# Kernel optimization log

Hardware: AMD Instinct MI355X
Metric: run time of the kernel (lower is better)

The kernel has to match this reference:

```python
import jax, jax.numpy as jnp
import numpy as np

DEPTH = 3  # node_info_propagator_stack_depth


def _gru_cell(x, h, W_ih, W_hh, b_ih, b_hh):
    # torch.nn.GRUCell math; x = input, h = hidden state
    gx = x @ W_ih.T + b_ih          # [..., 3P]
    gh = h @ W_hh.T + b_hh
    xr, xz, xn = jnp.split(gx, 3, axis=-1)
    hr, hz, hn = jnp.split(gh, 3, axis=-1)
    r = jax.nn.sigmoid(xr + hr)
    z = jax.nn.sigmoid(xz + hz)
    n = jnp.tanh(xn + r * hn)
    return (1.0 - z) * n + z * h


def setup_inputs() -> dict:
    key = jax.random.key(0)
    ks = jax.random.split(key, 16)
    B, N, E, P, C = 16, 4096, 256, 256, 8
    x = jax.random.normal(ks[0], (B, N, E), dtype=jnp.float32)
    parent_idx = jax.random.randint(ks[1], (B, N), 0, N, dtype=jnp.int32)
    children_idx = jax.random.randint(ks[2], (B, N, C), 0, N, dtype=jnp.int32)
    child_count = jax.random.randint(ks[3], (B, N), 1, C + 1, dtype=jnp.int32)

    def w(k, shape, fan_in):
        return jax.random.uniform(k, shape, dtype=jnp.float32,
                                  minval=-1.0, maxval=1.0) / np.sqrt(fan_in)

    return {
        "nodeInfosTensor": x,
        "parent_idx": parent_idx,
        "children_idx": children_idx,
        "child_count": child_count,
        "W_resize": w(ks[4], (P, E), E), "b_resize": w(ks[5], (P,), E),
        "W_parent": w(ks[6], (P, P), P), "b_parent": w(ks[7], (P,), P),
        "W_nbr": w(ks[8], (P, P), P), "b_nbr": w(ks[9], (P,), P),
        "W_ih": w(ks[10], (3 * P, P), P), "W_hh": w(ks[11], (3 * P, P), P),
        "b_ih": w(ks[12], (3 * P,), P), "b_hh": w(ks[13], (3 * P,), P),
    }


def reference(nodeInfosTensor, parent_idx, children_idx, child_count,
              W_resize, b_resize, W_parent, b_parent, W_nbr, b_nbr,
              W_ih, W_hh, b_ih, b_hh):
    h = nodeInfosTensor @ W_resize.T + b_resize          # [B,N,P]
    B, N, P = h.shape
    C = children_idx.shape[-1]
    # mask out padded child slots; original sums real children then /= count
    mask = (jnp.arange(C)[None, None, :] < child_count[:, :, None]).astype(h.dtype)
    inv_count = 1.0 / child_count.astype(h.dtype)        # count >= 1
    flat_children = children_idx.reshape(B, N * C)
    for _ in range(DEPTH):
        parent_info = jnp.take_along_axis(h, parent_idx[:, :, None], axis=1)  # [B,N,P]
        child_info = jnp.take_along_axis(h, flat_children[:, :, None], axis=1)
        child_info = child_info.reshape(B, N, C, P)
        nbr_info = (child_info * mask[..., None]).sum(axis=2) * inv_count[:, :, None]
        summary = (parent_info @ W_parent.T + b_parent) + (nbr_info @ W_nbr.T + b_nbr)
        # gruCell(input=h, hidden=summary)
        h = _gru_cell(h, summary, W_ih, W_hh, b_ih, b_hh)
    return h
```

## Files before the change

kernel.cpp:

```cpp
#include <hip/hip_runtime.h>

typedef unsigned short us;
typedef us us4 __attribute__((ext_vector_type(4)));
typedef us us8 __attribute__((ext_vector_type(8)));
typedef short bf16x8 __attribute__((ext_vector_type(8)));
typedef float f32x4 __attribute__((ext_vector_type(4)));

#define DEVI static __device__ __forceinline__

#define BB 16
#define NN 4096
#define PP 256
#define CC 8
#define MM (BB * NN)

DEVI float bf2f(us u) { unsigned x = ((unsigned)u) << 16; return __builtin_bit_cast(float, x); }
DEVI us f2bf(float f) {
  unsigned x = __builtin_bit_cast(unsigned, f);
  x += 0x7fffu + ((x >> 16) & 1u);
  return (us)(x >> 16);
}

DEVI void gload_lds16(const void* g, void* l) {
  __builtin_amdgcn_global_load_lds(
      (const __attribute__((address_space(1))) void*)g,
      (__attribute__((address_space(3))) void*)l, 16, 0, 0);
}

DEVI float sigf(float x) { return 1.f / (1.f + __expf(-x)); }
DEVI float tanhfast(float a) {
  float aa = fabsf(a);
  float t = 1.f - 2.f / (1.f + __expf(2.f * aa));
  return copysignf(t, a);
}

DEVI void raw_barrier() {
  __builtin_amdgcn_sched_barrier(0);
  __builtin_amdgcn_s_barrier();
  __builtin_amdgcn_sched_barrier(0);
}

__global__ void k_prep(const float* __restrict__ Wres,
                       const float* __restrict__ Wpar, const float* __restrict__ bpar,
                       const float* __restrict__ Wnbr, const float* __restrict__ bnbr,
                       const float* __restrict__ Wih, const float* __restrict__ Whh,
                       const float* __restrict__ bih, const float* __restrict__ bhh,
                       us* __restrict__ Wr, us* __restrict__ Wcat, float* __restrict__ bcat,
                       us* __restrict__ Wgh, us* __restrict__ Wgs, float* __restrict__ bg) {
  int tid = blockIdx.x * blockDim.x + threadIdx.x;
  int nth = gridDim.x * blockDim.x;
  for (int i = tid; i < 256 * 256; i += nth) Wr[i] = f2bf(Wres[i]);
  for (int i = tid; i < 256 * 512; i += nth) {
    int o = i >> 9, k = i & 511;
    float v = (k < 256) ? Wpar[o * 256 + k] : Wnbr[o * 256 + (k - 256)];
    Wcat[i] = f2bf(v);
  }
  for (int i = tid; i < 256; i += nth) bcat[i] = bpar[i] + bnbr[i];
  for (int i = tid; i < 768 * 256; i += nth) {
    int R = i >> 8, k = i & 255;
    int j = (R / 48) * 16 + (R & 15);
    int slot = (R >> 4) % 3;
    Wgh[i] = f2bf(Wih[(size_t)(slot * 256 + j) * 256 + k]);
    Wgs[i] = f2bf(Whh[(size_t)(slot * 256 + j) * 256 + k]);
  }
  for (int i = tid; i < 1024; i += nth) {
    int g = (i >> 4) & 3, j = ((i >> 6) << 4) + (i & 15);
    float v;
    if (g == 0)      v = bih[j] + bhh[j];
    else if (g == 1) v = bih[256 + j] + bhh[256 + j];
    else if (g == 2) v = bih[512 + j];
    else             v = bhh[512 + j];
    bg[i] = v;
  }
}

DEVI void mma8(const us* As, const us* Bs, int wr, int wc, int l,
               f32x4 (&acc)[8][4]) {
#pragma unroll
  for (int ks = 0; ks < 2; ++ks) {
    bf16x8 af[8], bfr[4];
#pragma unroll
    for (int i = 0; i < 8; ++i) {
      int row = wr * 128 + i * 16 + (l & 15);
      int kb = ((ks * 32 + (l >> 4) * 8) * 2) ^ ((row & 7) << 4);
      af[i] = *(const bf16x8*)((const char*)As + row * 128 + kb);
    }
#pragma unroll
    for (int j = 0; j < 4; ++j) {
      int row = wc * 64 + j * 16 + (l & 15);
      int kb = ((ks * 32 + (l >> 4) * 8) * 2) ^ ((row & 7) << 4);
      bfr[j] = *(const bf16x8*)((const char*)Bs + row * 128 + kb);
    }
#pragma unroll
    for (int i = 0; i < 8; ++i)
#pragma unroll
      for (int j = 0; j < 4; ++j)
        acc[i][j] = __builtin_amdgcn_mfma_f32_16x16x32_bf16(af[i], bfr[j], acc[i][j], 0, 0, 0);
  }
}

template <int HN, int KS>
DEVI void mma4g_ks(const us* As, const us* Bs, int wr, int wc, int l,
                   f32x4 (&acc)[4][4]) {
  bf16x8 af[4], bfr[3];
#pragma unroll
  for (int i = 0; i < 4; ++i) {
    int row = wr * 64 + i * 16 + (l & 15);
    int kb = ((KS * 32 + (l >> 4) * 8) * 2) ^ ((row & 7) << 4);
    af[i] = *(const bf16x8*)((const char*)As + row * 128 + kb);
  }
#pragma unroll
  for (int j = 0; j < 3; ++j) {
    int row = wc * 48 + j * 16 + (l & 15);
    int kb = ((KS * 32 + (l >> 4) * 8) * 2) ^ ((row & 7) << 4);
    bfr[j] = *(const bf16x8*)((const char*)Bs + row * 128 + kb);
  }
  __builtin_amdgcn_s_setprio(1);
#pragma unroll
  for (int i = 0; i < 4; ++i)
#pragma unroll
    for (int j = 0; j < 3; ++j) {
      int aj = (j < 2) ? j : (HN ? 3 : 2);
      acc[i][aj] = __builtin_amdgcn_mfma_f32_16x16x32_bf16(af[i], bfr[j], acc[i][aj], 0, 0, 0);
    }
  __builtin_amdgcn_s_setprio(0);
}

__global__ __launch_bounds__(512, 2)
void k_gemm0(const float* __restrict__ x, const us* __restrict__ Bw,
             const float* __restrict__ bias, us* __restrict__ outBf) {
  __shared__ __align__(16) us As[256 * 64];
  __shared__ __align__(16) us Bs[256 * 64];
  int tid = threadIdx.x;
  int w = tid >> 6, l = tid & 63;
  int wr = w >> 2, wc = w & 3;
  int bid = blockIdx.x;
  int per = gridDim.x >> 3;
  int mi = (bid & 7) * per + (bid >> 3);
  int mBase = mi * 256;
  f32x4 acc[8][4] = {};

#pragma unroll
  for (int t = 0; t < 4; ++t) {
    int kt = t * 64;
#pragma unroll
    for (int c = 0; c < 4; ++c) {
      int row = c * 64 + (tid >> 3);
      int kbb = ((tid & 7) * 16) ^ ((row & 7) << 4);
      const float* src = x + (size_t)(mBase + row) * 256 + kt + (kbb >> 1);
      float4 a = *(const float4*)src;
      float4 b = *(const float4*)(src + 4);
      us8 v;
      v[0] = f2bf(a.x); v[1] = f2bf(a.y); v[2] = f2bf(a.z); v[3] = f2bf(a.w);
      v[4] = f2bf(b.x); v[5] = f2bf(b.y); v[6] = f2bf(b.z); v[7] = f2bf(b.w);
      *(us8*)((char*)As + row * 128 + (tid & 7) * 16) = v;
      int kb = ((tid & 7) * 16) ^ ((row & 7) << 4);
      gload_lds16((const char*)(Bw + (size_t)row * 256 + kt) + kb,
                  (char*)Bs + row * 128 + (tid & 7) * 16);
    }
    asm volatile("s_waitcnt vmcnt(0)" ::: "memory");
    __syncthreads();
    mma8(As, Bs, wr, wc, l, acc);
    __syncthreads();
  }

  int rBase0 = mBase + wr * 128;
  int cBase0 = wc * 64;
#pragma unroll
  for (int i = 0; i < 8; ++i)
#pragma unroll
    for (int j = 0; j < 4; ++j) {
      int col = cBase0 + j * 16 + (l & 15);
      int row0 = rBase0 + i * 16 + ((l >> 4) << 2);
      float bb = bias[col];
#pragma unroll
      for (int e = 0; e < 4; ++e)
        outBf[(size_t)(row0 + e) * 256 + col] = f2bf(acc[i][j][e] + bb);
    }
}

__global__ __launch_bounds__(512, 2)
void k_sgemm(const us* __restrict__ h, const int* __restrict__ par,
             const int* __restrict__ chd, const int* __restrict__ cnt,
             const us* __restrict__ Wcat, const float* __restrict__ bcat,
             us* __restrict__ outBf, float* __restrict__ outF, int writeF32) {
  __shared__ __align__(16) us As[2][256 * 64];
  __shared__ __align__(16) us Bs[2][256 * 64];
  int tid = threadIdx.x;
  int w = tid >> 6, l = tid & 63;
  int wr = w >> 2, wc = w & 3;
  int bid = blockIdx.x;
  int per = gridDim.x >> 3;
  int mi = (bid & 7) * per + (bid >> 3);
  int mBase = mi * 256;
  int bb = (mBase >> 12) << 12;
  f32x4 acc[8][4] = {};

  int prow[4];
#pragma unroll
  for (int c = 0; c < 4; ++c)
    prow[c] = bb + par[mBase + c * 64 + (tid >> 3)];

  auto stageB = [&](int t) {
    int kt = t * 64, buf = t & 1;
#pragma unroll
    for (int c = 0; c < 4; ++c) {
      int row = c * 64 + (tid >> 3);
      int kb = ((tid & 7) * 16) ^ ((row & 7) << 4);
      gload_lds16((const char*)(Wcat + (size_t)row * 512 + kt) + kb,
                  (char*)Bs[buf] + row * 128 + (tid & 7) * 16);
    }
  };
  auto stageG = [&](int t) {
    int kt = t * 64, buf = t & 1;
#pragma unroll
    for (int c = 0; c < 4; ++c) {
      int row = c * 64 + (tid >> 3);
      int kb = ((tid & 7) * 16) ^ ((row & 7) << 4);
      gload_lds16((const char*)(h + (size_t)prow[c] * 256 + kt) + kb,
                  (char*)As[buf] + row * 128 + (tid & 7) * 16);
    }
    stageB(t);
  };
  auto stageN = [&](int t) {
    int kt = t * 64, buf = t & 1;
    int kOffBase = kt - 256;
#pragma unroll
    for (int c = 0; c < 4; ++c) {
      int row = c * 64 + (tid >> 3);
      int m = mBase + row;
      int kbb = ((tid & 7) * 16) ^ ((row & 7) << 4);
      const us* hb = h + (size_t)bb * 256 + kOffBase + (kbb >> 1);
      int4 c0 = *(const int4*)(chd + (size_t)m * CC);
      int4 c1 = *(const int4*)(chd + (size_t)m * CC + 4);
      int ci[8] = {c0.x, c0.y, c0.z, c0.w, c1.x, c1.y, c1.z, c1.w};
      int cn = cnt[m];
      float aa[8] = {0.f, 0.f, 0.f, 0.f, 0.f, 0.f, 0.f, 0.f};
#pragma unroll
      for (int r2 = 0; r2 < 2; ++r2) {
        us8 cv[4];
#pragma unroll
        for (int i2 = 0; i2 < 4; ++i2)
          cv[i2] = *(const us8*)(hb + (size_t)ci[r2 * 4 + i2] * 256);
#pragma unroll
        for (int i2 = 0; i2 < 4; ++i2) {
          float wgt = (r2 * 4 + i2 < cn) ? 1.f : 0.f;
#pragma unroll
          for (int e = 0; e < 8; ++e) aa[e] += wgt * bf2f(cv[i2][e]);
        }
      }
      float inv = 1.f / (float)cn;
      us8 nb;
#pragma unroll
      for (int e = 0; e < 8; ++e) nb[e] = f2bf(aa[e] * inv);
      *(us8*)((char*)As[buf] + row * 128 + (tid & 7) * 16) = nb;
    }
    asm volatile("s_waitcnt lgkmcnt(0)" ::: "memory");
    stageB(t);
  };

  stageG(0);
#pragma unroll
  for (int t = 0; t < 8; ++t) {
    if (t + 1 < 8) {
      if (t + 1 < 4) stageG(t + 1);
      else           stageN(t + 1);
    }
    if (t + 1 < 4)      asm volatile("s_waitcnt vmcnt(8)" ::: "memory");
    else if (t < 7)     asm volatile("s_waitcnt vmcnt(4)" ::: "memory");
    else                asm volatile("s_waitcnt vmcnt(0)" ::: "memory");
    raw_barrier();
    mma8(As[t & 1], Bs[t & 1], wr, wc, l, acc);
    raw_barrier();
  }

  int rBase0 = mBase + wr * 128;
  int cBase0 = wc * 64;
#pragma unroll
  for (int i = 0; i < 8; ++i)
#pragma unroll
    for (int j = 0; j < 4; ++j) {
      int col = cBase0 + j * 16 + (l & 15);
      int row0 = rBase0 + i * 16 + ((l >> 4) << 2);
      float bbia = bcat[col];
#pragma unroll
      for (int e = 0; e < 4; ++e) {
        float v = acc[i][j][e] + bbia;
        size_t off = (size_t)(row0 + e) * 256 + col;
        outBf[off] = f2bf(v);
        if (writeF32) outF[off] = v;
      }
    }
}

__global__ __launch_bounds__(512, 2)
void k_gates(const us* __restrict__ h, const us* __restrict__ s,
             const us* __restrict__ Wgh, const us* __restrict__ Wgs,
             const float* __restrict__ bg,
             us* __restrict__ outBf, float* __restrict__ outF,
             const us* __restrict__ svBf, const float* __restrict__ sF,
             int finalIt) {
  __shared__ __align__(16) us As[2][128 * 64];
  __shared__ __align__(16) us Bs[2][192 * 64];
  int tid = threadIdx.x;
  int w = tid >> 6, l = tid & 63;
  int wr = w >> 2, wc = w & 3;
  int bid = blockIdx.x;
  int per = gridDim.x >> 3;
  int g = (bid & 7) * per + (bid >> 3);
  int mi = g >> 2, ni = g & 3;
  int mBase = mi * 128, nB = ni * 192, nBase = ni * 256;
  f32x4 acc[4][4] = {};

  auto stageA = [&](int t) {
    int buf = t & 1;
    const us* aSrc = (t < 4) ? h : s;
    int kOff = (t & 3) * 64;
#pragma unroll
    for (int c = 0; c < 2; ++c) {
      int row = c * 64 + (tid >> 3);
      int kb = ((tid & 7) * 16) ^ ((row & 7) << 4);
      gload_lds16((const char*)(aSrc + (size_t)(mBase + row) * 256 + kOff) + kb,
                  (char*)As[buf] + row * 128 + (tid & 7) * 16);
    }
  };
  auto stageBw = [&](int t) {
    int buf = t & 1;
    const us* bSrc = (t < 4) ? Wgh : Wgs;
    int kOff = (t & 3) * 64;
#pragma unroll
    for (int c = 0; c < 3; ++c) {
      int row = c * 64 + (tid >> 3);
      int kb = ((tid & 7) * 16) ^ ((row & 7) << 4);
      gload_lds16((const char*)(bSrc + (size_t)(nB + row) * 256 + kOff) + kb,
                  (char*)Bs[buf] + row * 128 + (tid & 7) * 16);
    }
  };

  stageA(0); stageBw(0);
#pragma unroll
  for (int t = 0; t < 8; ++t) {
    if (t + 1 < 8) {
      stageA(t + 1); stageBw(t + 1);
      asm volatile("s_waitcnt vmcnt(5)" ::: "memory");
    } else {
      asm volatile("s_waitcnt vmcnt(0)" ::: "memory");
    }
    raw_barrier();
    const us* A = As[t & 1];
    const us* B = Bs[t & 1];
    if (t < 4) {
      mma4g_ks<0, 0>(A, B, wr, wc, l, acc);
      mma4g_ks<0, 1>(A, B, wr, wc, l, acc);
    } else {
      mma4g_ks<1, 0>(A, B, wr, wc, l, acc);
      mma4g_ks<1, 1>(A, B, wr, wc, l, acc);
    }
    raw_barrier();
  }

  int rBase0 = mBase + wr * 64;
  int cB = nBase + wc * 64;
  int outCol = ((nBase >> 6) + wc) * 16 + (l & 15);
  float b0 = bg[cB + 0  + (l & 15)];
  float b1 = bg[cB + 16 + (l & 15)];
  float b2 = bg[cB + 32 + (l & 15)];
  float b3 = bg[cB + 48 + (l & 15)];
#pragma unroll
  for (int i = 0; i < 4; ++i) {
    int row0 = rBase0 + i * 16 + ((l >> 4) << 2);
#pragma unroll
    for (int e = 0; e < 4; ++e) {
      float r = sigf(acc[i][0][e] + b0);
      float z = sigf(acc[i][1][e] + b1);
      float n = tanhfast(acc[i][2][e] + b2 + r * (acc[i][3][e] + b3));
      size_t off = (size_t)(row0 + e) * 256 + outCol;
      float sv = finalIt ? sF[off] : bf2f(svBf[off]);
      float o = (1.f - z) * n + z * sv;
      if (finalIt) outF[off] = o;
      else         outBf[off] = f2bf(o);
    }
  }
}

extern "C" void kernel_launch(void* const* d_in, const int* in_sizes, int n_in,
                              void* d_out, int out_size, void* d_ws, size_t ws_size,
                              hipStream_t stream) {
  const float* x    = (const float*)d_in[0];
  const int*   par  = (const int*)d_in[1];
  const int*   chd  = (const int*)d_in[2];
  const int*   cnt  = (const int*)d_in[3];
  const float* Wres = (const float*)d_in[4];
  const float* bres = (const float*)d_in[5];
  const float* Wpar = (const float*)d_in[6];
  const float* bpar = (const float*)d_in[7];
  const float* Wnbr = (const float*)d_in[8];
  const float* bnbr = (const float*)d_in[9];
  const float* Wih  = (const float*)d_in[10];
  const float* Whh  = (const float*)d_in[11];
  const float* bih  = (const float*)d_in[12];
  const float* bhh  = (const float*)d_in[13];

  char* ws = (char*)d_ws;
  size_t off = 0;
  auto alloc = [&](size_t sz) { char* p = ws + off; off += (sz + 255) & ~(size_t)255; return p; };
  us*    Wgh  = (us*)alloc((size_t)768 * 256 * 2);
  us*    Wgs  = (us*)alloc((size_t)768 * 256 * 2);
  us*    Wcat = (us*)alloc((size_t)256 * 512 * 2);
  us*    Wr   = (us*)alloc((size_t)256 * 256 * 2);
  float* bcat = (float*)alloc(256 * 4);
  float* bg   = (float*)alloc(1024 * 4);
  us*    sbf  = (us*)alloc((size_t)MM * 256 * 2);
  us*    h0   = (us*)alloc((size_t)MM * 256 * 2);
  us*    h1   = (us*)alloc((size_t)MM * 256 * 2);
  float* sF   = (float*)d_out;

  k_prep<<<256, 256, 0, stream>>>(Wres, Wpar, bpar, Wnbr, bnbr, Wih, Whh, bih, bhh,
                                  Wr, Wcat, bcat, Wgh, Wgs, bg);

  k_gemm0<<<256, 512, 0, stream>>>(x, Wr, bres, h0);

  us* hc = h0;
  for (int it = 0; it < 3; ++it) {
    us* hn = (hc == h0) ? h1 : h0;
    k_sgemm<<<256, 512, 0, stream>>>(hc, par, chd, cnt, Wcat, bcat,
                                     sbf, sF, (it == 2) ? 1 : 0);
    k_gates<<<2048, 512, 0, stream>>>(
        hc, sbf, Wgh, Wgs, bg, hn, (float*)d_out, sbf, sF, (it == 2) ? 1 : 0);
    hc = hn;
  }
}
```

Baseline: 386.0 us.

## Shrink summary GEMM tile to 128x128 and split N across blocks

After: 411.7 us. 1.07x slower.

```diff
diff --git a/kernel.cpp b/kernel.cpp
--- a/kernel.cpp
+++ b/kernel.cpp
@@ -99,6 +99,33 @@
   }
 }
 
+DEVI void mma_s(const us* As, const us* Bs, int wr, int wc, int l,
+                f32x4 (&acc)[4][2]) {
+#pragma unroll
+  for (int ks = 0; ks < 2; ++ks) {
+    bf16x8 af[4], bfr[2];
+#pragma unroll
+    for (int i = 0; i < 4; ++i) {
+      int row = wr * 64 + i * 16 + (l & 15);
+      int kb = ((ks * 32 + (l >> 4) * 8) * 2) ^ ((row & 7) << 4);
+      af[i] = *(const bf16x8*)((const char*)As + row * 128 + kb);
+    }
+#pragma unroll
+    for (int j = 0; j < 2; ++j) {
+      int row = wc * 32 + j * 16 + (l & 15);
+      int kb = ((ks * 32 + (l >> 4) * 8) * 2) ^ ((row & 7) << 4);
+      bfr[j] = *(const bf16x8*)((const char*)Bs + row * 128 + kb);
+    }
+    __builtin_amdgcn_s_setprio(1);
+#pragma unroll
+    for (int i = 0; i < 4; ++i)
+#pragma unroll
+      for (int j = 0; j < 2; ++j)
+        acc[i][j] = __builtin_amdgcn_mfma_f32_16x16x32_bf16(af[i], bfr[j], acc[i][j], 0, 0, 0);
+    __builtin_amdgcn_s_setprio(0);
+  }
+}
+
 template <int HN, int KS>
 DEVI void mma4g_ks(const us* As, const us* Bs, int wr, int wc, int l,
                    f32x4 (&acc)[4][4]) {
@@ -184,37 +211,38 @@
              const int* __restrict__ chd, const int* __restrict__ cnt,
              const us* __restrict__ Wcat, const float* __restrict__ bcat,
              us* __restrict__ outBf, float* __restrict__ outF, int writeF32) {
-  __shared__ __align__(16) us As[2][256 * 64];
-  __shared__ __align__(16) us Bs[2][256 * 64];
+  __shared__ __align__(16) us As[2][128 * 64];
+  __shared__ __align__(16) us Bs[2][128 * 64];
   int tid = threadIdx.x;
   int w = tid >> 6, l = tid & 63;
   int wr = w >> 2, wc = w & 3;
   int bid = blockIdx.x;
   int per = gridDim.x >> 3;
-  int mi = (bid & 7) * per + (bid >> 3);
-  int mBase = mi * 256;
+  int g = (bid & 7) * per + (bid >> 3);
+  int mi = g >> 1, ni = g & 1;
+  int mBase = mi * 128, nBase = ni * 128;
   int bb = (mBase >> 12) << 12;
-  f32x4 acc[8][4] = {};
-
-  int prow[4];
-#pragma unroll
-  for (int c = 0; c < 4; ++c)
+  f32x4 acc[4][2] = {};
+
+  int prow[2];
+#pragma unroll
+  for (int c = 0; c < 2; ++c)
     prow[c] = bb + par[mBase + c * 64 + (tid >> 3)];
 
   auto stageB = [&](int t) {
     int kt = t * 64, buf = t & 1;
 #pragma unroll
-    for (int c = 0; c < 4; ++c) {
+    for (int c = 0; c < 2; ++c) {
       int row = c * 64 + (tid >> 3);
       int kb = ((tid & 7) * 16) ^ ((row & 7) << 4);
-      gload_lds16((const char*)(Wcat + (size_t)row * 512 + kt) + kb,
+      gload_lds16((const char*)(Wcat + (size_t)(nBase + row) * 512 + kt) + kb,
                   (char*)Bs[buf] + row * 128 + (tid & 7) * 16);
     }
   };
   auto stageG = [&](int t) {
     int kt = t * 64, buf = t & 1;
 #pragma unroll
-    for (int c = 0; c < 4; ++c) {
+    for (int c = 0; c < 2; ++c) {
       int row = c * 64 + (tid >> 3);
       int kb = ((tid & 7) * 16) ^ ((row & 7) << 4);
       gload_lds16((const char*)(h + (size_t)prow[c] * 256 + kt) + kb,
@@ -226,7 +254,7 @@
     int kt = t * 64, buf = t & 1;
     int kOffBase = kt - 256;
 #pragma unroll
-    for (int c = 0; c < 4; ++c) {
+    for (int c = 0; c < 2; ++c) {
       int row = c * 64 + (tid >> 3);
       int m = mBase + row;
       int kbb = ((tid & 7) * 16) ^ ((row & 7) << 4);
@@ -266,20 +294,20 @@
       if (t + 1 < 4) stageG(t + 1);
       else           stageN(t + 1);
     }
-    if (t + 1 < 4)      asm volatile("s_waitcnt vmcnt(8)" ::: "memory");
-    else if (t < 7)     asm volatile("s_waitcnt vmcnt(4)" ::: "memory");
+    if (t + 1 < 4)      asm volatile("s_waitcnt vmcnt(4)" ::: "memory");
+    else if (t < 7)     asm volatile("s_waitcnt vmcnt(2)" ::: "memory");
     else                asm volatile("s_waitcnt vmcnt(0)" ::: "memory");
     raw_barrier();
-    mma8(As[t & 1], Bs[t & 1], wr, wc, l, acc);
+    mma_s(As[t & 1], Bs[t & 1], wr, wc, l, acc);
     raw_barrier();
   }
 
-  int rBase0 = mBase + wr * 128;
-  int cBase0 = wc * 64;
-#pragma unroll
-  for (int i = 0; i < 8; ++i)
-#pragma unroll
-    for (int j = 0; j < 4; ++j) {
+  int rBase0 = mBase + wr * 64;
+  int cBase0 = nBase + wc * 32;
+#pragma unroll
+  for (int i = 0; i < 4; ++i)
+#pragma unroll
+    for (int j = 0; j < 2; ++j) {
       int col = cBase0 + j * 16 + (l & 15);
       int row0 = rBase0 + i * 16 + ((l >> 4) << 2);
       float bbia = bcat[col];
@@ -423,8 +451,8 @@
   us* hc = h0;
   for (int it = 0; it < 3; ++it) {
     us* hn = (hc == h0) ? h1 : h0;
-    k_sgemm<<<256, 512, 0, stream>>>(hc, par, chd, cnt, Wcat, bcat,
-                                     sbf, sF, (it == 2) ? 1 : 0);
+    k_sgemm<<<1024, 512, 0, stream>>>(hc, par, chd, cnt, Wcat, bcat,
+                                      sbf, sF, (it == 2) ? 1 : 0);
     k_gates<<<2048, 512, 0, stream>>>(
         hc, sbf, Wgh, Wgs, bg, hn, (float*)d_out, sbf, sF, (it == 2) ? 1 : 0);
     hc = hn;
```
